# Kernel optimization log

Hardware: AMD Instinct MI355X
Metric: run time of the kernel (lower is better)

The kernel has to match this reference:

```python
import jax, jax.numpy as jnp
import numpy as np

CHANNELS = 512
NUM_HEADS = 8
GROUPS = 32
EPS = 1e-5


def setup_inputs() -> dict:
    key = jax.random.key(0)
    ks = jax.random.split(key, 7)
    C = CHANNELS
    x = jax.random.normal(ks[0], (8, C, 32, 32), dtype=jnp.float32)
    gn_weight = jnp.ones((C,), dtype=jnp.float32)
    gn_bias = jnp.zeros((C,), dtype=jnp.float32)
    # Conv1d(C, 3C, k=1) weights ~ N(0, 0.02) per init_weights
    qkv_w = 0.02 * jax.random.normal(ks[1], (3 * C, C), dtype=jnp.float32)
    qkv_b = 0.01 * jax.random.normal(ks[2], (3 * C,), dtype=jnp.float32)
    out_w = 0.02 * jax.random.normal(ks[3], (C, C), dtype=jnp.float32)
    out_b = 0.01 * jax.random.normal(ks[4], (C,), dtype=jnp.float32)
    return {"x": x, "gn_weight": gn_weight, "gn_bias": gn_bias,
            "qkv_w": qkv_w, "qkv_b": qkv_b, "out_w": out_w, "out_b": out_b}


def _forward(x, gn_weight, gn_bias, qkv_w, qkv_b, out_w, out_b):
    n, c, h, w = x.shape
    hw = h * w
    heads = NUM_HEADS
    cph = c // heads
    xs = x.reshape(n, c, hw)  # [N, C, HW]
    # GroupNorm over (channels-in-group, spatial)
    xg = xs.reshape(n, GROUPS, c // GROUPS, hw)
    mean = jnp.mean(xg, axis=(2, 3), keepdims=True)
    var = jnp.var(xg, axis=(2, 3), keepdims=True)
    xn = ((xg - mean) * jax.lax.rsqrt(var + EPS)).reshape(n, c, hw)
    xn = xn * gn_weight[None, :, None] + gn_bias[None, :, None]
    # 1x1 Conv1d QKV projection
    qkv = jnp.einsum('oc,ncl->nol', qkv_w, xn) + qkv_b[None, :, None]  # [N, 3C, HW]
    q, k, v = jnp.split(qkv, 3, axis=1)  # each [N, C, HW]
    q = q.reshape(n * heads, cph, hw)
    k = k.reshape(n * heads, cph, hw)
    v = v.reshape(n * heads, cph, hw)
    scale = 1.0 / np.sqrt(cph).astype(np.float32)
    scores = jnp.einsum('bci,bcj->bij', q, k) * scale  # [NH, HW, HW]
    attn = jax.nn.softmax(scores, axis=-1)
    weighted = jnp.einsum('bij,bcj->bic', attn, v)  # [NH, HW, cph]
    # Faithful to torch: reshape(n, -1, h, w) on [n*heads, hw, cph] layout
    weighted = weighted.reshape(n, c, h, w)
    out = jnp.einsum('oc,nchw->nohw', out_w, weighted) + out_b[None, :, None, None]
    return out


def reference(x, gn_weight, gn_bias, qkv_w, qkv_b, out_w, out_b):
    return _forward(x, gn_weight, gn_bias, qkv_w, qkv_b, out_w, out_b)
```

## Files before the change

### kernel.cpp

```cpp
#include <hip/hip_runtime.h>
#include <math.h>

#define N_    8
#define C_    512
#define HW_   1024
#define G_    32
#define CPG_  16
#define OC3_  1536
#define LOG2E 1.44269504f

typedef _Float16 f16;
typedef f16 f16x8 __attribute__((ext_vector_type(8)));
typedef f16 f16x4 __attribute__((ext_vector_type(4)));
typedef float f32x4 __attribute__((ext_vector_type(4)));

#define GLOAD_LDS16(g, l)                                                          \
    __builtin_amdgcn_global_load_lds(                                              \
        (const __attribute__((address_space(1))) unsigned int*)(const void*)(g),   \
        (__attribute__((address_space(3))) unsigned int*)(void*)(l), 16, 0, 0)

#define WAIT_VM0() __builtin_amdgcn_s_waitcnt(0x0F70)

__global__ __launch_bounds__(256) void prep(const float* __restrict__ x,
                                            const float* __restrict__ gw,
                                            const float* __restrict__ gb,
                                            f16* __restrict__ XT,
                                            const float* __restrict__ qkv_w,
                                            const float* __restrict__ out_w,
                                            const float* __restrict__ qkv_b,
                                            f16* __restrict__ Wq,
                                            f16* __restrict__ Wo,
                                            float* __restrict__ qkv_bs) {
    __shared__ float red1[4], red2[4];
    __shared__ float sm, srstd;
    if (blockIdx.x >= 256) {
        const float QS = 0.125f * LOG2E;
        int idx = (blockIdx.x - 256) * 256 + threadIdx.x;
        if (idx < 786432) {
            float v = qkv_w[idx];
            if (idx < 262144) v *= QS;
            Wq[idx] = (f16)v;
        } else if (idx < 786432 + 262144) {
            Wo[idx - 786432] = (f16)out_w[idx - 786432];
        } else if (idx < 786432 + 262144 + 1536) {
            int i = idx - 786432 - 262144;
            float v = qkv_b[i];
            if (i < 512) v *= QS;
            qkv_bs[i] = v;
        }
        return;
    }
    int blk = blockIdx.x;
    int n = blk >> 5, g = blk & 31;
    size_t base = ((size_t)n * C_ + (size_t)g * CPG_) * HW_;
    const float4* xp4 = (const float4*)(x + base);
    float4 vals[16];
    float s1 = 0.f, s2 = 0.f;
#pragma unroll
    for (int r = 0; r < 16; r++) {
        float4 v = xp4[r * 256 + threadIdx.x];
        vals[r] = v;
        s1 += v.x + v.y + v.z + v.w;
        s2 += v.x * v.x + v.y * v.y + v.z * v.z + v.w * v.w;
    }
#pragma unroll
    for (int off = 32; off > 0; off >>= 1) {
        s1 += __shfl_down(s1, off, 64);
        s2 += __shfl_down(s2, off, 64);
    }
    int wave = threadIdx.x >> 6, lane = threadIdx.x & 63;
    if (lane == 0) { red1[wave] = s1; red2[wave] = s2; }
    __syncthreads();
    if (threadIdx.x == 0) {
        float t1 = red1[0] + red1[1] + red1[2] + red1[3];
        float t2 = red2[0] + red2[1] + red2[2] + red2[3];
        float mean = t1 * (1.f / 16384.f);
        float var  = t2 * (1.f / 16384.f) - mean * mean;
        sm = mean;
        srstd = rsqrtf(var + 1e-5f);
    }
    __syncthreads();
    float mean = sm, rstd = srstd;
    float av[16], bbv[16];
#pragma unroll
    for (int r = 0; r < 16; r++) {
        int c = g * CPG_ + r;
        av[r] = gw[c] * rstd;
        bbv[r] = gb[c] - mean * av[r];
    }
    f16x8 lo[4], hi[4];
#pragma unroll
    for (int r = 0; r < 16; r++) {
        float4 v = vals[r];
        float a = av[r], bb = bbv[r];
        f16 e0 = (f16)(v.x * a + bb), e1 = (f16)(v.y * a + bb);
        f16 e2 = (f16)(v.z * a + bb), e3 = (f16)(v.w * a + bb);
        if (r < 8) { lo[0][r] = e0; lo[1][r] = e1; lo[2][r] = e2; lo[3][r] = e3; }
        else { hi[0][r - 8] = e0; hi[1][r - 8] = e1; hi[2][r - 8] = e2; hi[3][r - 8] = e3; }
    }
    f16* xt = XT + (size_t)n * C_ * HW_ + ((size_t)g * HW_ + threadIdx.x * 4) * 16;
#pragma unroll
    for (int comp = 0; comp < 4; comp++) {
        *(f16x8*)&xt[comp * 16]     = lo[comp];
        *(f16x8*)&xt[comp * 16 + 8] = hi[comp];
    }
}

template <bool FINAL>
__global__ __launch_bounds__(256, 4) void gemm_f16(const f16* __restrict__ A,
                                                   const f16* __restrict__ B,
                                                   const float* __restrict__ bias,
                                                   void* __restrict__ Yq,
                                                   f16* __restrict__ Yv) {
    __shared__ __align__(16) unsigned char smem[34816];
    f16* As = (f16*)smem;
    f16* Bs = (f16*)(smem + 16384);
    int tid = threadIdx.x, lane = tid & 63, w = tid >> 6;
    int m = lane & 15, quad = lane >> 4;
    int ow0 = (w & 1) * 64, lw0 = (w >> 1) * 64;
    int flat = blockIdx.x;
    int n = flat & 7, rest = flat >> 3;
    int l0 = (rest & 7) * 128, o0 = (rest >> 3) * 128;
    const f16* Bn = B + (size_t)n * C_ * HW_;

    int rowT[4], sgT[4];
#pragma unroll
    for (int t = 0; t < 4; t++) {
        int q = (w * 4 + t) * 64 + lane;
        int row = q >> 3, seg = q & 7;
        rowT[t] = row;
        sgT[t] = seg ^ (row & 7);
    }

    f32x4 acc[4][4];
#pragma unroll
    for (int i = 0; i < 4; i++)
#pragma unroll
        for (int j = 0; j < 4; j++)
#pragma unroll
            for (int r = 0; r < 4; r++) acc[i][j][r] = 0.f;

    for (int c0 = 0; c0 < 512; c0 += 64) {
        __syncthreads();
#pragma unroll
        for (int t = 0; t < 4; t++) {
            GLOAD_LDS16(A + (size_t)(o0 + rowT[t]) * 512 + c0 + sgT[t] * 8,
                        As + (size_t)(w * 4 + t) * 512);
            size_t baddr;
            if (FINAL) {
                baddr = (size_t)(l0 + rowT[t]) * 512 + c0 + sgT[t] * 8;
            } else {
                int c = c0 + sgT[t] * 8;
                baddr = ((size_t)(c >> 4) * HW_ + (l0 + rowT[t])) * 16 + (c & 15);
            }
            GLOAD_LDS16(Bn + baddr, Bs + (size_t)(w * 4 + t) * 512);
        }
        WAIT_VM0();
        __syncthreads();
#pragma unroll
        for (int ks = 0; ks < 2; ks++) {
            f16x8 af[4], bf[4];
#pragma unroll
            for (int ib = 0; ib < 4; ib++) {
                int row = ow0 + ib * 16 + m;
                int seg = (ks * 4 + quad) ^ (row & 7);
                af[ib] = *(const f16x8*)&As[row * 64 + seg * 8];
            }
#pragma unroll
            for (int jb = 0; jb < 4; jb++) {
                int row = lw0 + jb * 16 + m;
                int seg = (ks * 4 + quad) ^ (row & 7);
                bf[jb] = *(const f16x8*)&Bs[row * 64 + seg * 8];
            }
#pragma unroll
            for (int ib = 0; ib < 4; ib++)
#pragma unroll
                for (int jb = 0; jb < 4; jb++)
                    acc[ib][jb] = __builtin_amdgcn_mfma_f32_16x16x32_f16(
                        af[ib], bf[jb], acc[ib][jb], 0, 0, 0);
        }
    }

    float bv[4][4];
#pragma unroll
    for (int ib = 0; ib < 4; ib++)
#pragma unroll
        for (int r = 0; r < 4; r++)
            bv[ib][r] = bias[o0 + ow0 + ib * 16 + quad * 4 + r];

    if (FINAL) {
        float* on = (float*)Yq + (size_t)n * C_ * HW_;
#pragma unroll
        for (int ib = 0; ib < 4; ib++)
#pragma unroll
            for (int jb = 0; jb < 4; jb++)
#pragma unroll
                for (int r = 0; r < 4; r++)
                    on[(size_t)(o0 + ow0 + ib * 16 + quad * 4 + r) * HW_ +
                       l0 + lw0 + jb * 16 + m] = acc[ib][jb][r] + bv[ib][r];
    } else if (o0 >= 1024) {
        f16* vn = Yv + (size_t)n * C_ * HW_;
#pragma unroll
        for (int ib = 0; ib < 4; ib++)
#pragma unroll
            for (int jb = 0; jb < 4; jb++)
#pragma unroll
                for (int r = 0; r < 4; r++)
                    vn[(size_t)(o0 - 1024 + ow0 + ib * 16 + quad * 4 + r) * HW_ +
                       l0 + lw0 + jb * 16 + m] = (f16)(acc[ib][jb][r] + bv[ib][r]);
    } else {
        __syncthreads();
        f16* T = (f16*)smem;
#pragma unroll
        for (int ib = 0; ib < 4; ib++)
#pragma unroll
            for (int jb = 0; jb < 4; jb++) {
                f16x4 h;
#pragma unroll
                for (int r = 0; r < 4; r++) h[r] = (f16)(acc[ib][jb][r] + bv[ib][r]);
                int l = lw0 + jb * 16 + m;
                int oo = ow0 + ib * 16 + quad * 4;
                *(f16x4*)&T[l * 136 + oo] = h;
            }
        __syncthreads();
        f16* qn = (f16*)Yq + (size_t)n * HW_ * 1024;
#pragma unroll
        for (int rep = 0; rep < 8; rep++) {
            int idx = rep * 256 + tid;
            int l = idx >> 4, seg = idx & 15;
            f16x8 v = *(const f16x8*)&T[l * 136 + seg * 8];
            *(f16x8*)&qn[(size_t)(l0 + l) * 1024 + o0 + seg * 8] = v;
        }
    }
}

__global__ __launch_bounds__(256, 3) void attn_f16(const f16* __restrict__ qkvT,
                                                   const f16* __restrict__ vbuf,
                                                   f16* __restrict__ w2T) {
    __shared__ __align__(16) unsigned char smem[49152];
    f16* Kb0  = (f16*)smem;
    f16* Vb0  = (f16*)(smem + 16384);
    f16* Ps   = (f16*)(smem + 32768);
    f16* LDSo = (f16*)smem;

    int tid = threadIdx.x;
    int lane = tid & 63, wave = tid >> 6;
    int m = lane & 15, quad = lane >> 4;
    int flat = blockIdx.x;
    int xcd = flat & 7, slot = flat >> 3;
    int itile = slot >> 3, bh = (slot & 7) * 8 + xcd;
    int n = bh >> 3, head = bh & 7;
    int i0 = itile * 128;
    const f16* qb = qkvT + (size_t)n * HW_ * 1024 + head * 64;
    const f16* kb = qb + 512;
    const f16* vb = vbuf + (size_t)n * C_ * HW_ + (size_t)head * 64 * HW_;

    f16x8 aq[2][2];
#pragma unroll
    for (int s = 0; s < 2; s++) {
        const f16* qr = qb + (size_t)(i0 + wave * 32 + s * 16 + m) * 1024;
        aq[s][0] = *(const f16x8*)&qr[quad * 8];
        aq[s][1] = *(const f16x8*)&qr[32 + quad * 8];
    }

#pragma unroll
    for (int it = 0; it < 2; it++) {
        int chunk = it * 256 + tid;
        int row = chunk >> 3, seg = chunk & 7;
        int segg = seg ^ (row & 7);
        GLOAD_LDS16(kb + (size_t)row * 1024 + segg * 8,
                    Kb0 + ((size_t)it * 256 + wave * 64) * 8);
        GLOAD_LDS16(vb + (size_t)row * HW_ + segg * 8,
                    Vb0 + ((size_t)it * 256 + wave * 64) * 8);
    }

    f32x4 oacc[2][4];
#pragma unroll
    for (int s = 0; s < 2; s++)
#pragma unroll
        for (int cb = 0; cb < 4; cb++)
#pragma unroll
            for (int r = 0; r < 4; r++) oacc[s][cb][r] = 0.f;
    float lsum[2] = {0.f, 0.f};

    for (int jt = 0; jt < 16; jt++) {
        int p = jt & 1;
        const f16* Kp = Kb0 + p * 4096;
        const f16* Vp = Vb0 + p * 4096;
        WAIT_VM0();
        __syncthreads();
        if (jt < 15) {
            int j0n = (jt + 1) * 64;
            f16* Kn = Kb0 + (1 - p) * 4096;
            f16* Vn = Vb0 + (1 - p) * 4096;
#pragma unroll
            for (int it = 0; it < 2; it++) {
                int chunk = it * 256 + tid;
                int row = chunk >> 3, seg = chunk & 7;
                int segg = seg ^ (row & 7);
                GLOAD_LDS16(kb + (size_t)(j0n + row) * 1024 + segg * 8,
                            Kn + ((size_t)it * 256 + wave * 64) * 8);
                GLOAD_LDS16(vb + (size_t)row * HW_ + j0n + segg * 8,
                            Vn + ((size_t)it * 256 + wave * 64) * 8);
            }
        }

        f16x8 kf[8], vf[8];
#pragma unroll
        for (int jb = 0; jb < 4; jb++) {
            int row = jb * 16 + m;
            kf[jb]     = *(const f16x8*)&Kp[row * 64 + ((quad ^ (row & 7)) * 8)];
            kf[4 + jb] = *(const f16x8*)&Kp[row * 64 + (((4 + quad) ^ (row & 7)) * 8)];
            vf[jb]     = *(const f16x8*)&Vp[row * 64 + ((quad ^ (row & 7)) * 8)];
            vf[4 + jb] = *(const f16x8*)&Vp[row * 64 + (((4 + quad) ^ (row & 7)) * 8)];
        }

#pragma unroll
        for (int s = 0; s < 2; s++) {
            f16* PsW = Ps + (size_t)(wave * 2 + s) * 1024;
            f32x4 sacc[4];
#pragma unroll
            for (int jb = 0; jb < 4; jb++)
#pragma unroll
                for (int r = 0; r < 4; r++) sacc[jb][r] = 0.f;
#pragma unroll
            for (int jb = 0; jb < 4; jb++)
                sacc[jb] = __builtin_amdgcn_mfma_f32_16x16x32_f16(kf[jb], aq[s][0],
                                                                  sacc[jb], 0, 0, 0);
#pragma unroll
            for (int jb = 0; jb < 4; jb++)
                sacc[jb] = __builtin_amdgcn_mfma_f32_16x16x32_f16(kf[4 + jb], aq[s][1],
                                                                  sacc[jb], 0, 0, 0);

#pragma unroll
            for (int jb = 0; jb < 4; jb++) {
                f16x4 h;
#pragma unroll
                for (int r = 0; r < 4; r++) {
                    float pv = exp2f(sacc[jb][r]);
                    h[r] = (f16)pv;
                    lsum[s] += pv;
                }
                int seg = jb * 4 + quad;
                *(f16x4*)&PsW[m * 64 + ((seg ^ (m & 7)) * 4)] = h;
            }

#pragma unroll
            for (int ks = 0; ks < 2; ks++) {
                int s0 = ks * 8 + quad * 2;
                f16x4 apl = *(const f16x4*)&PsW[m * 64 + ((s0 ^ (m & 7)) * 4)];
                f16x4 aph = *(const f16x4*)&PsW[m * 64 + (((s0 + 1) ^ (m & 7)) * 4)];
                f16x8 ap = {apl[0], apl[1], apl[2], apl[3],
                            aph[0], aph[1], aph[2], aph[3]};
#pragma unroll
                for (int cb = 0; cb < 4; cb++)
                    oacc[s][cb] = __builtin_amdgcn_mfma_f32_16x16x32_f16(
                        ap, vf[ks * 4 + cb], oacc[s][cb], 0, 0, 0);
            }
        }
    }

    float linv[2][4];
#pragma unroll
    for (int s = 0; s < 2; s++) {
        float ls = lsum[s];
        ls += __shfl_xor(ls, 16, 64);
        ls += __shfl_xor(ls, 32, 64);
#pragma unroll
        for (int r = 0; r < 4; r++)
            linv[s][r] = 1.f / __shfl(ls, quad * 4 + r, 64);
    }
    WAIT_VM0();
    __syncthreads();
#pragma unroll
    for (int s = 0; s < 2; s++)
#pragma unroll
        for (int cb = 0; cb < 4; cb++)
#pragma unroll
            for (int r = 0; r < 4; r++) {
                int sc = (quad * 4 + r) * 64 + cb * 16 + m;
                LDSo[sc * 8 + wave * 2 + s] = (f16)(oacc[s][cb][r] * linv[s][r]);
            }
    __syncthreads();
    f16* w2n = w2T + (size_t)n * HW_ * 512;
    int chbase = head * 64 + (i0 >> 4);
#pragma unroll
    for (int it = 0; it < 4; it++) {
        int sc = it * 256 + tid;
        *(f16x8*)&w2n[(size_t)sc * 512 + chbase] = *(const f16x8*)&LDSo[sc * 8];
    }
}

extern "C" void kernel_launch(void* const* d_in, const int* in_sizes, int n_in,
                              void* d_out, int out_size, void* d_ws, size_t ws_size,
                              hipStream_t stream) {
    (void)in_sizes; (void)n_in; (void)out_size; (void)ws_size;
    const float* x     = (const float*)d_in[0];
    const float* gw    = (const float*)d_in[1];
    const float* gb    = (const float*)d_in[2];
    const float* qkv_w = (const float*)d_in[3];
    const float* qkv_b = (const float*)d_in[4];
    const float* out_w = (const float*)d_in[5];
    const float* out_b = (const float*)d_in[6];
    float* out = (float*)d_out;
    char* ws = (char*)d_ws;

    const size_t MB = 1024 * 1024;
    f16*   qkvT   = (f16*)ws;
    f16*   XT     = (f16*)(ws + 16 * MB);
    f16*   vbuf   = (f16*)(ws + 24 * MB);
    f16*   w2T    = (f16*)(ws + 32 * MB);
    f16*   Wq     = (f16*)(ws + 40 * MB);
    f16*   Wo     = (f16*)(ws + 42 * MB);
    float* qkv_bs = (float*)(ws + 43 * MB);

    prep<<<dim3(256 + 4103), 256, 0, stream>>>(x, gw, gb, XT,
                                               qkv_w, out_w, qkv_b, Wq, Wo, qkv_bs);
    gemm_f16<false><<<dim3(768), 256, 0, stream>>>(Wq, XT, qkv_bs, (void*)qkvT, vbuf);
    attn_f16<<<dim3(512), 256, 0, stream>>>(qkvT, vbuf, w2T);
    gemm_f16<true><<<dim3(256), 256, 0, stream>>>(Wo, w2T, out_b, (void*)out, nullptr);
}
```

Measured before the change: 153.4 us.

## Keep softmax probabilities in registers and halve attention query tile

The attention kernel now feeds the exp'd score fragments straight into a 16x16x16 MFMA as the A operand, so the LDS round trip for P goes away and the 16 KB P buffer is dropped. Each block handles 64 queries instead of 128, the grid doubles to 1024 blocks, and occupancy is raised to 4 blocks per CU. The trade is that K/V tiles are now loaded twice as often in total across blocks, V fragments are re-read from LDS per jb, and the smaller-K MFMA instruction is used for PV. Output writes shrink to 4-element vectors.

```diff
diff --git a/kernel.cpp b/kernel.cpp
--- a/kernel.cpp
+++ b/kernel.cpp
@@ -234,13 +234,12 @@
     }
 }
 
-__global__ __launch_bounds__(256, 3) void attn_f16(const f16* __restrict__ qkvT,
+__global__ __launch_bounds__(256, 4) void attn_f16(const f16* __restrict__ qkvT,
                                                    const f16* __restrict__ vbuf,
                                                    f16* __restrict__ w2T) {
-    __shared__ __align__(16) unsigned char smem[49152];
+    __shared__ __align__(16) unsigned char smem[32768];
     f16* Kb0  = (f16*)smem;
     f16* Vb0  = (f16*)(smem + 16384);
-    f16* Ps   = (f16*)(smem + 32768);
     f16* LDSo = (f16*)smem;
 
     int tid = threadIdx.x;
@@ -250,18 +249,14 @@
     int xcd = flat & 7, slot = flat >> 3;
     int itile = slot >> 3, bh = (slot & 7) * 8 + xcd;
     int n = bh >> 3, head = bh & 7;
-    int i0 = itile * 128;
+    int i0 = itile * 64;
     const f16* qb = qkvT + (size_t)n * HW_ * 1024 + head * 64;
     const f16* kb = qb + 512;
     const f16* vb = vbuf + (size_t)n * C_ * HW_ + (size_t)head * 64 * HW_;
 
-    f16x8 aq[2][2];
-#pragma unroll
-    for (int s = 0; s < 2; s++) {
-        const f16* qr = qb + (size_t)(i0 + wave * 32 + s * 16 + m) * 1024;
-        aq[s][0] = *(const f16x8*)&qr[quad * 8];
-        aq[s][1] = *(const f16x8*)&qr[32 + quad * 8];
-    }
+    const f16* qr = qb + (size_t)(i0 + wave * 16 + m) * 1024;
+    f16x8 aq0 = *(const f16x8*)&qr[quad * 8];
+    f16x8 aq1 = *(const f16x8*)&qr[32 + quad * 8];
 
 #pragma unroll
     for (int it = 0; it < 2; it++) {
@@ -274,14 +269,13 @@
                     Vb0 + ((size_t)it * 256 + wave * 64) * 8);
     }
 
-    f32x4 oacc[2][4];
-#pragma unroll
-    for (int s = 0; s < 2; s++)
-#pragma unroll
-        for (int cb = 0; cb < 4; cb++)
-#pragma unroll
-            for (int r = 0; r < 4; r++) oacc[s][cb][r] = 0.f;
-    float lsum[2] = {0.f, 0.f};
+    f32x4 oacc[4];
+#pragma unroll
+    for (int cb = 0; cb < 4; cb++)
+#pragma unroll
+        for (int r = 0; r < 4; r++) oacc[cb][r] = 0.f;
+    float lsum = 0.f;
+    int m7 = m & 7;
 
     for (int jt = 0; jt < 16; jt++) {
         int p = jt & 1;
@@ -305,89 +299,74 @@
             }
         }
 
-        f16x8 kf[8], vf[8];
+        f16x8 kf[8];
 #pragma unroll
         for (int jb = 0; jb < 4; jb++) {
             int row = jb * 16 + m;
             kf[jb]     = *(const f16x8*)&Kp[row * 64 + ((quad ^ (row & 7)) * 8)];
             kf[4 + jb] = *(const f16x8*)&Kp[row * 64 + (((4 + quad) ^ (row & 7)) * 8)];
-            vf[jb]     = *(const f16x8*)&Vp[row * 64 + ((quad ^ (row & 7)) * 8)];
-            vf[4 + jb] = *(const f16x8*)&Vp[row * 64 + (((4 + quad) ^ (row & 7)) * 8)];
-        }
-
-#pragma unroll
-        for (int s = 0; s < 2; s++) {
-            f16* PsW = Ps + (size_t)(wave * 2 + s) * 1024;
-            f32x4 sacc[4];
-#pragma unroll
-            for (int jb = 0; jb < 4; jb++)
-#pragma unroll
-                for (int r = 0; r < 4; r++) sacc[jb][r] = 0.f;
-#pragma unroll
-            for (int jb = 0; jb < 4; jb++)
-                sacc[jb] = __builtin_amdgcn_mfma_f32_16x16x32_f16(kf[jb], aq[s][0],
-                                                                  sacc[jb], 0, 0, 0);
-#pragma unroll
-            for (int jb = 0; jb < 4; jb++)
-                sacc[jb] = __builtin_amdgcn_mfma_f32_16x16x32_f16(kf[4 + jb], aq[s][1],
-                                                                  sacc[jb], 0, 0, 0);
-
-#pragma unroll
-            for (int jb = 0; jb < 4; jb++) {
-                f16x4 h;
-#pragma unroll
-                for (int r = 0; r < 4; r++) {
-                    float pv = exp2f(sacc[jb][r]);
-                    h[r] = (f16)pv;
-                    lsum[s] += pv;
-                }
-                int seg = jb * 4 + quad;
-                *(f16x4*)&PsW[m * 64 + ((seg ^ (m & 7)) * 4)] = h;
-            }
-
-#pragma unroll
-            for (int ks = 0; ks < 2; ks++) {
-                int s0 = ks * 8 + quad * 2;
-                f16x4 apl = *(const f16x4*)&PsW[m * 64 + ((s0 ^ (m & 7)) * 4)];
-                f16x4 aph = *(const f16x4*)&PsW[m * 64 + (((s0 + 1) ^ (m & 7)) * 4)];
-                f16x8 ap = {apl[0], apl[1], apl[2], apl[3],
-                            aph[0], aph[1], aph[2], aph[3]};
-#pragma unroll
-                for (int cb = 0; cb < 4; cb++)
-                    oacc[s][cb] = __builtin_amdgcn_mfma_f32_16x16x32_f16(
-                        ap, vf[ks * 4 + cb], oacc[s][cb], 0, 0, 0);
-            }
-        }
-    }
-
-    float linv[2][4];
-#pragma unroll
-    for (int s = 0; s < 2; s++) {
-        float ls = lsum[s];
-        ls += __shfl_xor(ls, 16, 64);
-        ls += __shfl_xor(ls, 32, 64);
-#pragma unroll
-        for (int r = 0; r < 4; r++)
-            linv[s][r] = 1.f / __shfl(ls, quad * 4 + r, 64);
-    }
+        }
+
+        f32x4 sacc[4];
+#pragma unroll
+        for (int jb = 0; jb < 4; jb++)
+#pragma unroll
+            for (int r = 0; r < 4; r++) sacc[jb][r] = 0.f;
+#pragma unroll
+        for (int jb = 0; jb < 4; jb++)
+            sacc[jb] = __builtin_amdgcn_mfma_f32_16x16x32_f16(kf[jb], aq0,
+                                                              sacc[jb], 0, 0, 0);
+#pragma unroll
+        for (int jb = 0; jb < 4; jb++)
+            sacc[jb] = __builtin_amdgcn_mfma_f32_16x16x32_f16(kf[4 + jb], aq1,
+                                                              sacc[jb], 0, 0, 0);
+
+        f16x4 pf[4];
+#pragma unroll
+        for (int jb = 0; jb < 4; jb++) {
+            float p0 = exp2f(sacc[jb][0]), p1 = exp2f(sacc[jb][1]);
+            float p2 = exp2f(sacc[jb][2]), p3 = exp2f(sacc[jb][3]);
+            lsum += (p0 + p1) + (p2 + p3);
+            pf[jb][0] = (f16)p0; pf[jb][1] = (f16)p1;
+            pf[jb][2] = (f16)p2; pf[jb][3] = (f16)p3;
+        }
+
+#pragma unroll
+        for (int jb = 0; jb < 4; jb++) {
+            int segb = jb * 2 + (quad >> 1);
+#pragma unroll
+            for (int cb = 0; cb < 4; cb++) {
+                f16x4 vf4 = *(const f16x4*)&Vp[(cb * 16 + m) * 64 +
+                                               ((segb ^ m7) * 8) + (quad & 1) * 4];
+                oacc[cb] = __builtin_amdgcn_mfma_f32_16x16x16f16(pf[jb], vf4,
+                                                                 oacc[cb], 0, 0, 0);
+            }
+        }
+    }
+
+    float ls = lsum;
+    ls += __shfl_xor(ls, 16, 64);
+    ls += __shfl_xor(ls, 32, 64);
+    float linv[4];
+#pragma unroll
+    for (int r = 0; r < 4; r++) linv[r] = 1.f / __shfl(ls, quad * 4 + r, 64);
+
     WAIT_VM0();
     __syncthreads();
 #pragma unroll
-    for (int s = 0; s < 2; s++)
-#pragma unroll
-        for (int cb = 0; cb < 4; cb++)
-#pragma unroll
-            for (int r = 0; r < 4; r++) {
-                int sc = (quad * 4 + r) * 64 + cb * 16 + m;
-                LDSo[sc * 8 + wave * 2 + s] = (f16)(oacc[s][cb][r] * linv[s][r]);
-            }
+    for (int cb = 0; cb < 4; cb++)
+#pragma unroll
+        for (int r = 0; r < 4; r++) {
+            int sc = (quad * 4 + r) * 64 + cb * 16 + m;
+            LDSo[sc * 4 + wave] = (f16)(oacc[cb][r] * linv[r]);
+        }
     __syncthreads();
     f16* w2n = w2T + (size_t)n * HW_ * 512;
     int chbase = head * 64 + (i0 >> 4);
 #pragma unroll
     for (int it = 0; it < 4; it++) {
         int sc = it * 256 + tid;
-        *(f16x8*)&w2n[(size_t)sc * 512 + chbase] = *(const f16x8*)&LDSo[sc * 8];
+        *(f16x4*)&w2n[(size_t)sc * 512 + chbase] = *(const f16x4*)&LDSo[sc * 4];
     }
 }
 
@@ -417,6 +396,6 @@
     prep<<<dim3(256 + 4103), 256, 0, stream>>>(x, gw, gb, XT,
                                                qkv_w, out_w, qkv_b, Wq, Wo, qkv_bs);
     gemm_f16<false><<<dim3(768), 256, 0, stream>>>(Wq, XT, qkv_bs, (void*)qkvT, vbuf);
-    attn_f16<<<dim3(512), 256, 0, stream>>>(qkvT, vbuf, w2T);
+    attn_f16<<<dim3(1024), 256, 0, stream>>>(qkvT, vbuf, w2T);
     gemm_f16<true><<<dim3(256), 256, 0, stream>>>(Wo, w2T, out_b, (void*)out, nullptr);
 }
```

New measurement: 151.2 us. No clear change (-1.4%).
